# Kernel optimization log

Measured on AMD Instinct MI355X. Metric: run time of the kernel, lower is better.

## Reference

```python
import jax, jax.numpy as jnp
import numpy as np

D_MODEL = 40
NUM_BUCKETS = 32
MAX_DISTANCE = 128
EPS = 1e-6


def rms_norm(x, w):
    # T5 LayerNorm: no mean subtraction, no bias
    var = jnp.mean(jnp.square(x), axis=-1, keepdims=True)
    return x * jax.lax.rsqrt(var + EPS) * w


def relative_position_bucket(rel, num_buckets=NUM_BUCKETS, max_distance=MAX_DISTANCE):
    # bidirectional (encoder) variant of T5's bucketing
    num_buckets = num_buckets // 2
    buckets = (rel > 0).astype(jnp.int32) * num_buckets
    rel = jnp.abs(rel)
    max_exact = num_buckets // 2
    is_small = rel < max_exact
    rel_f = jnp.maximum(rel, 1).astype(jnp.float32)
    large = max_exact + (
        jnp.log(rel_f / max_exact) / np.log(max_distance / max_exact) * (num_buckets - max_exact)
    ).astype(jnp.int32)
    large = jnp.minimum(large, num_buckets - 1)
    return buckets + jnp.where(is_small, rel, large)


def setup_inputs() -> dict:
    key = jax.random.key(0)
    ks = jax.random.split(key, 16)
    B, S, Din, D = 8, 2048, 128, D_MODEL
    w = lambda k, shape: (jax.random.normal(k, shape, dtype=jnp.float32) * 0.02)
    return {
        "embs": jax.random.normal(ks[0], (B, S, Din), dtype=jnp.float32),
        "Wa": w(ks[1], (Din, D)),
        "ba": jnp.zeros((D,), dtype=jnp.float32),
        "ln1": jnp.ones((D,), dtype=jnp.float32),
        "Wq": w(ks[2], (D, D)),
        "Wk": w(ks[3], (D, D)),
        "Wv": w(ks[4], (D, D)),
        "Wo": w(ks[5], (D, D)),
        "ln2": jnp.ones((D,), dtype=jnp.float32),
        "wi": w(ks[6], (D, D)),
        "wo": w(ks[7], (D, D)),
        "lnf": jnp.ones((D,), dtype=jnp.float32),
        "rel_bias": w(ks[8], (NUM_BUCKETS, 1)),  # [num_buckets, n_heads=1]
    }


def reference(embs, Wa, ba, ln1, Wq, Wk, Wv, Wo, ln2, wi, wo, lnf, rel_bias):
    # adapter
    x = jax.nn.relu(embs @ Wa + ba)  # [B,S,D]
    S = x.shape[1]

    # --- self-attention block (1 head, d_kv = d_model, no QK scaling) ---
    h = rms_norm(x, ln1)
    q = h @ Wq  # [B,S,D]
    k = h @ Wk
    v = h @ Wv

    pos = jnp.arange(S)
    rel = pos[None, :] - pos[:, None]           # memory - query, [S,S]
    buckets = relative_position_bucket(rel)      # [S,S]
    pos_bias = rel_bias[buckets][:, :, 0]        # [S,S], head dim squeezed (1 head)

    scores = jnp.einsum("bqd,bkd->bqk", q, k) + pos_bias[None]  # [B,S,S]
    attn = jax.nn.softmax(scores, axis=-1)
    o = jnp.einsum("bqk,bkd->bqd", attn, v) @ Wo
    x = x + o

    # --- feed-forward block ---
    h2 = rms_norm(x, ln2)
    f = jax.nn.relu(h2 @ wi) @ wo
    x = x + f

    return rms_norm(x, lnf)
```

## Files before the change

kernel.cpp:

```cpp
#include <hip/hip_runtime.h>
#include <hip/hip_bf16.h>
#include <math.h>

#define D 40
#define DIN 128
#define S 2048
#define B 8
#define NROWS (B*S)
#define DP 64
#define XSTR 48
#define PSTR 64
#define KSTR 72

typedef __bf16 bf16x8 __attribute__((ext_vector_type(8)));
typedef float f32x16 __attribute__((ext_vector_type(16)));

static __device__ __forceinline__ unsigned short f2bf(float f) {
    unsigned u = __builtin_bit_cast(unsigned, f);
    u += 0x7fff + ((u >> 16) & 1);
    return (unsigned short)(u >> 16);
}
static __device__ __forceinline__ float bf2f(unsigned short h) {
    return __builtin_bit_cast(float, (unsigned)h << 16);
}
static __device__ __forceinline__ bf16x8 ldfrag(const unsigned short* p) {
    return __builtin_bit_cast(bf16x8, *(const uint4*)p);
}
static __device__ __forceinline__ unsigned cvtpk(float lo, float hi) {
    unsigned r;
    asm("v_cvt_pk_bf16_f32 %0, %1, %2" : "=v"(r) : "v"(lo), "v"(hi));
    return r;
}
static __device__ __forceinline__ void plswap(unsigned &a, unsigned &b) {
    asm("v_permlane32_swap_b32 %0, %1" : "+v"(a), "+v"(b));
}

__global__ __launch_bounds__(256) void k0_prep(
    const float* __restrict__ Wa, const float* __restrict__ ba, const float* __restrict__ ln1,
    const float* __restrict__ Wq, const float* __restrict__ Wk, const float* __restrict__ Wv,
    const float* __restrict__ Wo, const float* __restrict__ ln2,
    const float* __restrict__ wi, const float* __restrict__ wo,
    const float* __restrict__ rel_bias,
    unsigned short* __restrict__ waT, unsigned short* __restrict__ wqT,
    unsigned short* __restrict__ wkT, unsigned short* __restrict__ wvT,
    unsigned short* __restrict__ woT, unsigned short* __restrict__ wiT,
    unsigned short* __restrict__ wo2T, float* __restrict__ btab)
{
    int i = blockIdx.x * 256 + threadIdx.x;
    if (i < 64*144) {
        int col = i / 144, k = i - col*144;
        float v = 0.f;
        if (col < D) {
            if (k < DIN) v = Wa[k*D + col];
            else if (k == DIN) v = ba[col];
        }
        waT[i] = f2bf(v);
    }
    if (i < 64*48) {
        int col = i / 48, d = i - col*48;
        bool ok = (col < D && d < D);
        float s1 = ok ? ln1[d] : 0.f;
        float s2 = ok ? ln2[d] : 0.f;
        wqT[i]  = f2bf(ok ? Wq[d*D + col] * s1 : 0.f);
        wkT[i]  = f2bf(ok ? Wk[d*D + col] * s1 : 0.f);
        wvT[i]  = f2bf(ok ? Wv[d*D + col] * s1 : 0.f);
        woT[i]  = f2bf(ok ? Wo[d*D + col]      : 0.f);
        wiT[i]  = f2bf(ok ? wi[d*D + col] * s2 : 0.f);
        wo2T[i] = f2bf(ok ? wo[d*D + col]      : 0.f);
    }
    if (i < 2*S - 1) {
        int rel = i - (S - 1);
        int bucket = (rel > 0) ? 16 : 0;
        int ar = rel < 0 ? -rel : rel;
        int add;
        if (ar < 8) {
            add = ar;
        } else {
            float tt = logf((float)ar * 0.125f) / logf(16.0f) * 8.0f;
            int lg = 8 + (int)tt;
            add = lg < 15 ? lg : 15;
        }
        btab[i] = rel_bias[bucket + add];
    }
}

static __device__ __forceinline__ void repack1(const f32x16& t0, uint4& u0, uint4& u1)
{
    unsigned a0=cvtpk(t0[0],t0[1]),  a1=cvtpk(t0[2],t0[3]),
             a2=cvtpk(t0[4],t0[5]),  a3=cvtpk(t0[6],t0[7]);
    plswap(a0,a2); plswap(a1,a3);
    unsigned b0=cvtpk(t0[8],t0[9]),  b1=cvtpk(t0[10],t0[11]),
             b2=cvtpk(t0[12],t0[13]),b3=cvtpk(t0[14],t0[15]);
    plswap(b0,b2); plswap(b1,b3);
    u0 = (uint4){a0,a1,a2,a3}; u1 = (uint4){b0,b1,b2,b3};
}

__global__ __launch_bounds__(128) void k1_adapter_qkv(
    const float* __restrict__ embs,
    const unsigned short* __restrict__ waT, const unsigned short* __restrict__ wqT,
    const unsigned short* __restrict__ wkT, const unsigned short* __restrict__ wvT,
    unsigned short* __restrict__ xb, unsigned short* __restrict__ qb,
    unsigned short* __restrict__ kbq, unsigned short* __restrict__ vT)
{
    __shared__ __attribute__((aligned(16))) unsigned short sE16[32][136];
    __shared__ unsigned short sX[32][56];
    __shared__ float sSS[2][32];

    const int tid = threadIdx.x;

    {
        int r = tid >> 2;
        int cc = (tid & 3) * 32;
        const float* src = embs + (size_t)(blockIdx.x*32 + r) * DIN + cc;
        #pragma unroll
        for (int i = 0; i < 4; ++i) {
            float4 f0 = *(const float4*)(src + i*8);
            float4 f1 = *(const float4*)(src + i*8 + 4);
            uint4 u = { cvtpk(f0.x, f0.y), cvtpk(f0.z, f0.w),
                        cvtpk(f1.x, f1.y), cvtpk(f1.z, f1.w) };
            *(uint4*)&sE16[r][cc + i*8] = u;
        }
    }
    __syncthreads();

    const int w   = tid >> 6;
    const int l   = tid & 63;
    const int lr  = l & 31, hi = l >> 5;
    const int row = blockIdx.x * 32 + lr;
    const int cb  = w * 32;

    bf16x8 eb[9];
    #pragma unroll
    for (int kk = 0; kk < 8; ++kk) eb[kk] = ldfrag(&sE16[lr][kk*16 + hi*8]);
    {
        uint4 u = { hi == 0 ? 0x3f80u : 0u, 0u, 0u, 0u };
        eb[8] = __builtin_bit_cast(bf16x8, u);
    }

    f32x16 x0 = {0,0,0,0,0,0,0,0,0,0,0,0,0,0,0,0};
    #pragma unroll
    for (int kk = 0; kk < 9; ++kk) {
        bf16x8 a0 = ldfrag(waT + (size_t)(cb + lr)*144 + kk*16 + hi*8);
        x0 = __builtin_amdgcn_mfma_f32_32x32x16_bf16(a0, eb[kk], x0, 0,0,0);
    }

    float ss = 0.f;
    #pragma unroll
    for (int r = 0; r < 16; ++r) {
        x0[r] = fmaxf(x0[r], 0.f);
        ss += x0[r]*x0[r];
    }
    ss += __shfl_xor(ss, 32);
    if (hi == 0) sSS[w][lr] = ss;
    __syncthreads();
    const float inv = rsqrtf((sSS[0][lr] + sSS[1][lr]) * (1.0f/D) + 1e-6f);

    {
        uint4 u0, u1; repack1(x0, u0, u1);
        unsigned short* p = xb + (size_t)row*XSTR;
        *(uint4*)(p + cb + hi*8) = u0;
        if (w == 0) *(uint4*)(p + 16 + hi*8) = u1;
    }

    f32x16 xh;
    #pragma unroll
    for (int r = 0; r < 16; ++r) xh[r] = x0[r] * inv;
    {
        uint4 u0, u1; repack1(xh, u0, u1);
        *(uint4*)(&sX[lr][cb + hi*8]) = u0;
        if (w == 0) *(uint4*)(&sX[lr][16 + hi*8]) = u1;
    }
    __syncthreads();
    bf16x8 hb[3];
    #pragma unroll
    for (int t = 0; t < 3; ++t) hb[t] = ldfrag(&sX[lr][t*16 + hi*8]);

    f32x16 qa={0,0,0,0,0,0,0,0,0,0,0,0,0,0,0,0};
    f32x16 ka={0,0,0,0,0,0,0,0,0,0,0,0,0,0,0,0};
    f32x16 va={0,0,0,0,0,0,0,0,0,0,0,0,0,0,0,0};
    #pragma unroll
    for (int t = 0; t < 3; ++t) {
        bf16x8 h = hb[t];
        qa = __builtin_amdgcn_mfma_f32_32x32x16_bf16(ldfrag(wqT + (size_t)(cb+lr)*48 + t*16 + hi*8), h, qa, 0,0,0);
        ka = __builtin_amdgcn_mfma_f32_32x32x16_bf16(ldfrag(wkT + (size_t)(cb+lr)*48 + t*16 + hi*8), h, ka, 0,0,0);
        va = __builtin_amdgcn_mfma_f32_32x32x16_bf16(ldfrag(wvT + (size_t)(cb+lr)*48 + t*16 + hi*8), h, va, 0,0,0);
    }

    {
        uint4 u0, u1; repack1(qa, u0, u1);
        unsigned short* p = qb + (size_t)row*DP;
        *(uint4*)(p + cb + hi*8) = u0;
        if (w == 0) *(uint4*)(p + 16 + hi*8) = u1;
    }
    {
        uint4 u0, u1; repack1(ka, u0, u1);
        unsigned short* p = kbq + (size_t)row*DP;
        *(uint4*)(p + cb + hi*8) = u0;
        if (w == 0) *(uint4*)(p + 16 + hi*8) = u1;
    }
    #pragma unroll
    for (int r = 0; r < 16; ++r) {
        int col = cb + (r&3) + 8*(r>>2) + 4*hi;
        vT[(size_t)col*NROWS + row] = f2bf(va[r]);
    }
}

__global__ __launch_bounds__(256) void k3_attn_mfma(
    const unsigned short* __restrict__ qb, const unsigned short* __restrict__ kb,
    const unsigned short* __restrict__ vT, const float* __restrict__ btab,
    unsigned short* __restrict__ pob, float* __restrict__ pl, int klen, int nsplit)
{
    __shared__ float sbtw[2176 + 16];
    __shared__ __attribute__((aligned(16))) unsigned short sK[64][KSTR];
    __shared__ __attribute__((aligned(16))) unsigned short sV[64][KSTR];

    const int q0blk = blockIdx.x * 128;
    const int kt0   = blockIdx.z * klen;
    const int woff  = (S-1) + kt0 - q0blk - 127;

    int tid = threadIdx.x;
    for (int i = tid; i < klen + 128; i += 256) {
        int g = woff + i;
        sbtw[i] = btab[g < 0 ? 0 : (g > 4094 ? 4094 : g)];
    }

    const int w  = tid >> 6, l = tid & 63;
    const int lr = l & 31,  hi = l >> 5;
    const int b  = blockIdx.y;
    const int q0 = q0blk + w * 32;

    const unsigned short* qrow = qb + ((size_t)(b*S) + q0 + lr) * DP + hi*8;
    bf16x8 qf0 = ldfrag(qrow);
    bf16x8 qf1 = ldfrag(qrow + 16);
    bf16x8 qf2 = ldfrag(qrow + 32);

    f32x16 of0 = {0,0,0,0,0,0,0,0,0,0,0,0,0,0,0,0};
    f32x16 of1 = {0,0,0,0,0,0,0,0,0,0,0,0,0,0,0,0};
    float el = 0.f;

    const int bb = 127 - w*32 - lr + 4*hi;

    const int srow = tid >> 3;
    const int scol = (tid & 7) * 8;

    auto stageRegs = [&](int kc, uint4& rk0, uint4& rk1, uint4& rv0, uint4& rv1) {
        const unsigned short* src = kb + (size_t)(b*S + kt0 + kc)*DP;
        rk0 = *(const uint4*)(src + (size_t)srow*DP + scol);
        rk1 = *(const uint4*)(src + (size_t)(32 + srow)*DP + scol);
        const unsigned short* vsrc = vT + (size_t)(b*S) + kt0 + kc;
        rv0 = *(const uint4*)(vsrc + (size_t)srow*NROWS + scol);
        rv1 = *(const uint4*)(vsrc + (size_t)(32 + srow)*NROWS + scol);
    };
    auto writeLds = [&](const uint4& rk0, const uint4& rk1, const uint4& rv0, const uint4& rv1) {
        *(uint4*)&sK[srow][scol]      = rk0;
        *(uint4*)&sK[32 + srow][scol] = rk1;
        *(uint4*)&sV[srow][scol]      = rv0;
        *(uint4*)&sV[32 + srow][scol] = rv1;
    };

    auto compute = [&](int ktl, int kloc) {
        bf16x8 kf0 = ldfrag(&sK[kloc + lr][hi*8]);
        bf16x8 kf1 = ldfrag(&sK[kloc + lr][16 + hi*8]);
        bf16x8 kf2 = ldfrag(&sK[kloc + lr][32 + hi*8]);
        f32x16 c = {0,0,0,0,0,0,0,0,0,0,0,0,0,0,0,0};
        c = __builtin_amdgcn_mfma_f32_32x32x16_bf16(kf0, qf0, c, 0,0,0);
        c = __builtin_amdgcn_mfma_f32_32x32x16_bf16(kf1, qf1, c, 0,0,0);
        c = __builtin_amdgcn_mfma_f32_32x32x16_bf16(kf2, qf2, c, 0,0,0);

        float e[16];
        #pragma unroll
        for (int r = 0; r < 16; ++r) {
            float s = c[r] + sbtw[bb + ktl + (r&3) + 8*(r>>2)];
            e[r] = __expf(s);
            el += e[r];
        }
        unsigned a0 = cvtpk(e[0],  e[1]);
        unsigned a1 = cvtpk(e[2],  e[3]);
        unsigned a2 = cvtpk(e[4],  e[5]);
        unsigned a3 = cvtpk(e[6],  e[7]);
        plswap(a0, a2);
        plswap(a1, a3);
        unsigned b0 = cvtpk(e[8],  e[9]);
        unsigned b1 = cvtpk(e[10], e[11]);
        unsigned b2 = cvtpk(e[12], e[13]);
        unsigned b3 = cvtpk(e[14], e[15]);
        plswap(b0, b2);
        plswap(b1, b3);
        uint4 u0 = {a0, a1, a2, a3};
        uint4 u1 = {b0, b1, b2, b3};
        bf16x8 pa0 = __builtin_bit_cast(bf16x8, u0);
        bf16x8 pa1 = __builtin_bit_cast(bf16x8, u1);

        bf16x8 vf0 = ldfrag(&sV[lr][kloc + hi*8]);
        bf16x8 vf1 = ldfrag(&sV[lr][kloc + 16 + hi*8]);
        bf16x8 vf2 = ldfrag(&sV[32 + lr][kloc + hi*8]);
        bf16x8 vf3 = ldfrag(&sV[32 + lr][kloc + 16 + hi*8]);

        of0 = __builtin_amdgcn_mfma_f32_32x32x16_bf16(pa0, vf0, of0, 0,0,0);
        of0 = __builtin_amdgcn_mfma_f32_32x32x16_bf16(pa1, vf1, of0, 0,0,0);
        of1 = __builtin_amdgcn_mfma_f32_32x32x16_bf16(pa0, vf2, of1, 0,0,0);
        of1 = __builtin_amdgcn_mfma_f32_32x32x16_bf16(pa1, vf3, of1, 0,0,0);
    };

    {
        uint4 rk0, rk1, rv0, rv1;
        stageRegs(0, rk0, rk1, rv0, rv1);
        writeLds(rk0, rk1, rv0, rv1);
    }
    __syncthreads();

    for (int kc = 0; kc < klen; kc += 64) {
        const bool more = (kc + 64 < klen);
        uint4 rk0, rk1, rv0, rv1;
        if (more) stageRegs(kc + 64, rk0, rk1, rv0, rv1);
        compute(kc, 0);
        compute(kc + 32, 32);
        if (more) {
            __syncthreads();
            writeLds(rk0, rk1, rv0, rv1);
            __syncthreads();
        }
    }

    el += __shfl_xor(el, 32);

    const size_t rb0 = ((size_t)(b*S + q0) * nsplit + blockIdx.z);
    #pragma unroll
    for (int r = 0; r < 16; ++r) {
        int qr = (r&3) + 8*(r>>2) + 4*hi;
        unsigned short* pr = pob + (rb0 + (size_t)qr * nsplit) * PSTR;
        pr[lr] = f2bf(of0[r]);
        if (lr < 8) pr[32 + lr] = f2bf(of1[r]);
    }
    if (hi == 0) pl[(size_t)blockIdx.z * NROWS + b*S + q0 + lr] = el;
}

__global__ __launch_bounds__(128) void k4_out_ff(
    const unsigned short* __restrict__ xb, const unsigned short* __restrict__ pob,
    const float* __restrict__ pl,
    const unsigned short* __restrict__ woT, const unsigned short* __restrict__ wiT,
    const unsigned short* __restrict__ wo2T, const float* __restrict__ lnf,
    float* __restrict__ out, int nsplit)
{
    __shared__ unsigned short sX[32][56];
    __shared__ float sSS[2][32];

    const int tid = threadIdx.x;
    const int w   = tid >> 6;
    const int l   = tid & 63;
    const int lr  = l & 31, hi = l >> 5;
    const int row = blockIdx.x * 32 + lr;
    const int cb  = w * 32;

    float lsum = 0.f;
    for (int s = 0; s < nsplit; ++s) lsum += pl[(size_t)s*NROWS + row];
    const float linv = 1.0f / lsum;

    float a[3][8];
    #pragma unroll
    for (int t = 0; t < 3; ++t)
        #pragma unroll
        for (int j = 0; j < 8; ++j) a[t][j] = 0.f;
    const unsigned short* prow = pob + (size_t)row * nsplit * PSTR;
    for (int s = 0; s < nsplit; ++s) {
        const unsigned short* pr = prow + (size_t)s * PSTR;
        #pragma unroll
        for (int t = 0; t < 3; ++t) {
            if (t == 2 && hi == 1) continue;
            uint4 u = *(const uint4*)(pr + t*16 + hi*8);
            a[t][0] += bf2f((unsigned short)(u.x)); a[t][1] += bf2f((unsigned short)(u.x >> 16));
            a[t][2] += bf2f((unsigned short)(u.y)); a[t][3] += bf2f((unsigned short)(u.y >> 16));
            a[t][4] += bf2f((unsigned short)(u.z)); a[t][5] += bf2f((unsigned short)(u.z >> 16));
            a[t][6] += bf2f((unsigned short)(u.w)); a[t][7] += bf2f((unsigned short)(u.w >> 16));
        }
    }
    bf16x8 ab[3];
    #pragma unroll
    for (int t = 0; t < 3; ++t) {
        uint4 u = { cvtpk(a[t][0]*linv, a[t][1]*linv), cvtpk(a[t][2]*linv, a[t][3]*linv),
                    cvtpk(a[t][4]*linv, a[t][5]*linv), cvtpk(a[t][6]*linv, a[t][7]*linv) };
        ab[t] = __builtin_bit_cast(bf16x8, u);
    }

    f32x16 c = {0,0,0,0,0,0,0,0,0,0,0,0,0,0,0,0};
    #pragma unroll
    for (int t = 0; t < 3; ++t)
        c = __builtin_amdgcn_mfma_f32_32x32x16_bf16(ldfrag(woT + (size_t)(cb+lr)*48 + t*16 + hi*8), ab[t], c, 0,0,0);

    const unsigned short* xr = xb + (size_t)row*XSTR;
    if (w == 0) {
        #pragma unroll
        for (int rr = 0; rr < 4; ++rr) {
            ushort4 v = *(const ushort4*)(xr + rr*8 + 4*hi);
            c[rr*4+0] += bf2f(v.x); c[rr*4+1] += bf2f(v.y);
            c[rr*4+2] += bf2f(v.z); c[rr*4+3] += bf2f(v.w);
        }
    } else {
        ushort4 v = *(const ushort4*)(xr + 32 + 4*hi);
        c[0] += bf2f(v.x); c[1] += bf2f(v.y); c[2] += bf2f(v.z); c[3] += bf2f(v.w);
    }

    float ss = 0.f;
    #pragma unroll
    for (int r = 0; r < 16; ++r) ss += c[r]*c[r];
    ss += __shfl_xor(ss, 32);
    if (hi == 0) sSS[w][lr] = ss;
    __syncthreads();
    const float inv2 = rsqrtf((sSS[0][lr] + sSS[1][lr]) * (1.0f/D) + 1e-6f);

    f32x16 t0;
    #pragma unroll
    for (int r = 0; r < 16; ++r) t0[r] = c[r]*inv2;
    {
        uint4 u0, u1; repack1(t0, u0, u1);
        *(uint4*)(&sX[lr][cb + hi*8]) = u0;
        if (w == 0) *(uint4*)(&sX[lr][16 + hi*8]) = u1;
    }
    __syncthreads();
    bf16x8 hb[3];
    #pragma unroll
    for (int t = 0; t < 3; ++t) hb[t] = ldfrag(&sX[lr][t*16 + hi*8]);
    __syncthreads();

    f32x16 d = {0,0,0,0,0,0,0,0,0,0,0,0,0,0,0,0};
    #pragma unroll
    for (int t = 0; t < 3; ++t)
        d = __builtin_amdgcn_mfma_f32_32x32x16_bf16(ldfrag(wiT + (size_t)(cb+lr)*48 + t*16 + hi*8), hb[t], d, 0,0,0);
    #pragma unroll
    for (int r = 0; r < 16; ++r) d[r] = fmaxf(d[r], 0.f);
    {
        uint4 u0, u1; repack1(d, u0, u1);
        *(uint4*)(&sX[lr][cb + hi*8]) = u0;
        if (w == 0) *(uint4*)(&sX[lr][16 + hi*8]) = u1;
    }
    __syncthreads();
    bf16x8 fb[3];
    #pragma unroll
    for (int t = 0; t < 3; ++t) fb[t] = ldfrag(&sX[lr][t*16 + hi*8]);

    f32x16 e = {0,0,0,0,0,0,0,0,0,0,0,0,0,0,0,0};
    #pragma unroll
    for (int t = 0; t < 3; ++t)
        e = __builtin_amdgcn_mfma_f32_32x32x16_bf16(ldfrag(wo2T + (size_t)(cb+lr)*48 + t*16 + hi*8), fb[t], e, 0,0,0);
    #pragma unroll
    for (int r = 0; r < 16; ++r) e[r] += c[r];

    float ss2 = 0.f;
    #pragma unroll
    for (int r = 0; r < 16; ++r) ss2 += e[r]*e[r];
    ss2 += __shfl_xor(ss2, 32);
    if (hi == 0) sSS[w][lr] = ss2;
    __syncthreads();
    const float inv3 = rsqrtf((sSS[0][lr] + sSS[1][lr]) * (1.0f/D) + 1e-6f);

    float* orow = out + (size_t)row * D;
    if (w == 0) {
        #pragma unroll
        for (int rr = 0; rr < 4; ++rr) {
            float4 lf = *(const float4*)(lnf + rr*8 + 4*hi);
            float4 v = { e[rr*4+0]*inv3*lf.x, e[rr*4+1]*inv3*lf.y,
                         e[rr*4+2]*inv3*lf.z, e[rr*4+3]*inv3*lf.w };
            *(float4*)(orow + rr*8 + 4*hi) = v;
        }
    } else {
        float4 lf = *(const float4*)(lnf + 32 + 4*hi);
        float4 v = { e[0]*inv3*lf.x, e[1]*inv3*lf.y, e[2]*inv3*lf.z, e[3]*inv3*lf.w };
        *(float4*)(orow + 32 + 4*hi) = v;
    }
}

extern "C" void kernel_launch(void* const* d_in, const int* in_sizes, int n_in,
                              void* d_out, int out_size, void* d_ws, size_t ws_size,
                              hipStream_t stream) {
    const float* embs = (const float*)d_in[0];
    const float* Wa   = (const float*)d_in[1];
    const float* ba   = (const float*)d_in[2];
    const float* ln1  = (const float*)d_in[3];
    const float* Wq   = (const float*)d_in[4];
    const float* Wk   = (const float*)d_in[5];
    const float* Wv   = (const float*)d_in[6];
    const float* Wo   = (const float*)d_in[7];
    const float* ln2  = (const float*)d_in[8];
    const float* wi   = (const float*)d_in[9];
    const float* wo   = (const float*)d_in[10];
    const float* lnf  = (const float*)d_in[11];
    const float* rb   = (const float*)d_in[12];

    char* wsb = (char*)d_ws;
    unsigned short* xb   = (unsigned short*)(wsb);
    unsigned short* qb   = (unsigned short*)(wsb + 1572864);
    unsigned short* kbq  = (unsigned short*)(wsb + 3670016);
    unsigned short* vT   = (unsigned short*)(wsb + 5767168);
    unsigned short* waT  = (unsigned short*)(wsb + 7864320);
    unsigned short* wqT  = (unsigned short*)(wsb + 7882752);
    unsigned short* wkT  = (unsigned short*)(wsb + 7888896);
    unsigned short* wvT  = (unsigned short*)(wsb + 7895040);
    unsigned short* woT  = (unsigned short*)(wsb + 7901184);
    unsigned short* wiT  = (unsigned short*)(wsb + 7907328);
    unsigned short* wo2T = (unsigned short*)(wsb + 7913472);
    const size_t base = 7919616;

    int nsplit = 8;
    while (nsplit > 1 &&
           base + (size_t)nsplit*(2097152 + 65536) + 16384 > ws_size)
        nsplit >>= 1;
    unsigned short* pob = (unsigned short*)(wsb + base);
    float* pl   = (float*)(wsb + base + (size_t)nsplit*2097152);
    float* btab = (float*)(wsb + base + (size_t)nsplit*(2097152 + 65536));
    int klen = S / nsplit;

    k0_prep<<<36, 256, 0, stream>>>(Wa, ba, ln1, Wq, Wk, Wv, Wo, ln2, wi, wo, rb,
                                    waT, wqT, wkT, wvT, woT, wiT, wo2T, btab);
    k1_adapter_qkv<<<NROWS/32, 128, 0, stream>>>(embs, waT, wqT, wkT, wvT, xb, qb, kbq, vT);
    k3_attn_mfma<<<dim3(S/128, B, nsplit), 256, 0, stream>>>(qb, kbq, vT, btab, pob, pl, klen, nsplit);
    k4_out_ff<<<NROWS/32, 128, 0, stream>>>(xb, pob, pl, woT, wiT, wo2T, lnf, (float*)d_out, nsplit);
}
```

Baseline: 45.55 us.

## Process two query tiles per wave in attention kernel to reuse staged K/V

Each attention block now covers 256 query rows instead of 128. Each wave holds two sets of Q fragments and two sets of accumulators and runs both against every K/V tile staged in LDS. This halves the K/V global loads and LDS staging per query and halves the grid size. The cost is more registers per thread, which the launch bound of 2 blocks per CU tries to contain, and fewer blocks (with nsplit=8 it drops from 1024 to 512) to fill the CUs.

```diff
diff --git a/kernel.cpp b/kernel.cpp
--- a/kernel.cpp
+++ b/kernel.cpp
@@ -205,21 +205,21 @@
     }
 }
 
-__global__ __launch_bounds__(256) void k3_attn_mfma(
+__global__ __launch_bounds__(256, 2) void k3_attn_mfma(
     const unsigned short* __restrict__ qb, const unsigned short* __restrict__ kb,
     const unsigned short* __restrict__ vT, const float* __restrict__ btab,
     unsigned short* __restrict__ pob, float* __restrict__ pl, int klen, int nsplit)
 {
-    __shared__ float sbtw[2176 + 16];
+    __shared__ float sbtw[2432];
     __shared__ __attribute__((aligned(16))) unsigned short sK[64][KSTR];
     __shared__ __attribute__((aligned(16))) unsigned short sV[64][KSTR];
 
-    const int q0blk = blockIdx.x * 128;
+    const int q0blk = blockIdx.x * 256;
     const int kt0   = blockIdx.z * klen;
-    const int woff  = (S-1) + kt0 - q0blk - 127;
+    const int woff  = (S-1) + kt0 - q0blk - 255;
 
     int tid = threadIdx.x;
-    for (int i = tid; i < klen + 128; i += 256) {
+    for (int i = tid; i < klen + 256; i += 256) {
         int g = woff + i;
         sbtw[i] = btab[g < 0 ? 0 : (g > 4094 ? 4094 : g)];
     }
@@ -227,18 +227,22 @@
     const int w  = tid >> 6, l = tid & 63;
     const int lr = l & 31,  hi = l >> 5;
     const int b  = blockIdx.y;
-    const int q0 = q0blk + w * 32;
-
-    const unsigned short* qrow = qb + ((size_t)(b*S) + q0 + lr) * DP + hi*8;
-    bf16x8 qf0 = ldfrag(qrow);
-    bf16x8 qf1 = ldfrag(qrow + 16);
-    bf16x8 qf2 = ldfrag(qrow + 32);
-
-    f32x16 of0 = {0,0,0,0,0,0,0,0,0,0,0,0,0,0,0,0};
-    f32x16 of1 = {0,0,0,0,0,0,0,0,0,0,0,0,0,0,0,0};
-    float el = 0.f;
-
-    const int bb = 127 - w*32 - lr + 4*hi;
+    const int q0a = q0blk + w * 32;
+    const int q0b = q0a + 128;
+
+    const unsigned short* qrA = qb + ((size_t)(b*S) + q0a + lr) * DP + hi*8;
+    bf16x8 qfA[3] = { ldfrag(qrA), ldfrag(qrA + 16), ldfrag(qrA + 32) };
+    const unsigned short* qrB = qb + ((size_t)(b*S) + q0b + lr) * DP + hi*8;
+    bf16x8 qfB[3] = { ldfrag(qrB), ldfrag(qrB + 16), ldfrag(qrB + 32) };
+
+    f32x16 oA0 = {0,0,0,0,0,0,0,0,0,0,0,0,0,0,0,0};
+    f32x16 oA1 = {0,0,0,0,0,0,0,0,0,0,0,0,0,0,0,0};
+    f32x16 oB0 = {0,0,0,0,0,0,0,0,0,0,0,0,0,0,0,0};
+    f32x16 oB1 = {0,0,0,0,0,0,0,0,0,0,0,0,0,0,0,0};
+    float elA = 0.f, elB = 0.f;
+
+    const int bbA = 255 - w*32 - lr + 4*hi;
+    const int bbB = bbA - 128;
 
     const int srow = tid >> 3;
     const int scol = (tid & 7) * 8;
@@ -258,14 +262,15 @@
         *(uint4*)&sV[32 + srow][scol] = rv1;
     };
 
-    auto compute = [&](int ktl, int kloc) {
+    auto compute = [&](int ktl, int kloc, const bf16x8* qf,
+                       f32x16& o0, f32x16& o1, float& el, int bb) {
         bf16x8 kf0 = ldfrag(&sK[kloc + lr][hi*8]);
         bf16x8 kf1 = ldfrag(&sK[kloc + lr][16 + hi*8]);
         bf16x8 kf2 = ldfrag(&sK[kloc + lr][32 + hi*8]);
         f32x16 c = {0,0,0,0,0,0,0,0,0,0,0,0,0,0,0,0};
-        c = __builtin_amdgcn_mfma_f32_32x32x16_bf16(kf0, qf0, c, 0,0,0);
-        c = __builtin_amdgcn_mfma_f32_32x32x16_bf16(kf1, qf1, c, 0,0,0);
-        c = __builtin_amdgcn_mfma_f32_32x32x16_bf16(kf2, qf2, c, 0,0,0);
+        c = __builtin_amdgcn_mfma_f32_32x32x16_bf16(kf0, qf[0], c, 0,0,0);
+        c = __builtin_amdgcn_mfma_f32_32x32x16_bf16(kf1, qf[1], c, 0,0,0);
+        c = __builtin_amdgcn_mfma_f32_32x32x16_bf16(kf2, qf[2], c, 0,0,0);
 
         float e[16];
         #pragma unroll
@@ -296,10 +301,10 @@
         bf16x8 vf2 = ldfrag(&sV[32 + lr][kloc + hi*8]);
         bf16x8 vf3 = ldfrag(&sV[32 + lr][kloc + 16 + hi*8]);
 
-        of0 = __builtin_amdgcn_mfma_f32_32x32x16_bf16(pa0, vf0, of0, 0,0,0);
-        of0 = __builtin_amdgcn_mfma_f32_32x32x16_bf16(pa1, vf1, of0, 0,0,0);
-        of1 = __builtin_amdgcn_mfma_f32_32x32x16_bf16(pa0, vf2, of1, 0,0,0);
-        of1 = __builtin_amdgcn_mfma_f32_32x32x16_bf16(pa1, vf3, of1, 0,0,0);
+        o0 = __builtin_amdgcn_mfma_f32_32x32x16_bf16(pa0, vf0, o0, 0,0,0);
+        o0 = __builtin_amdgcn_mfma_f32_32x32x16_bf16(pa1, vf1, o0, 0,0,0);
+        o1 = __builtin_amdgcn_mfma_f32_32x32x16_bf16(pa0, vf2, o1, 0,0,0);
+        o1 = __builtin_amdgcn_mfma_f32_32x32x16_bf16(pa1, vf3, o1, 0,0,0);
     };
 
     {
@@ -313,8 +318,10 @@
         const bool more = (kc + 64 < klen);
         uint4 rk0, rk1, rv0, rv1;
         if (more) stageRegs(kc + 64, rk0, rk1, rv0, rv1);
-        compute(kc, 0);
-        compute(kc + 32, 32);
+        compute(kc,      0,  qfA, oA0, oA1, elA, bbA);
+        compute(kc,      0,  qfB, oB0, oB1, elB, bbB);
+        compute(kc + 32, 32, qfA, oA0, oA1, elA, bbA);
+        compute(kc + 32, 32, qfB, oB0, oB1, elB, bbB);
         if (more) {
             __syncthreads();
             writeLds(rk0, rk1, rv0, rv1);
@@ -322,17 +329,25 @@
         }
     }
 
-    el += __shfl_xor(el, 32);
-
-    const size_t rb0 = ((size_t)(b*S + q0) * nsplit + blockIdx.z);
+    elA += __shfl_xor(elA, 32);
+    elB += __shfl_xor(elB, 32);
+
+    const size_t rbA = ((size_t)(b*S + q0a) * nsplit + blockIdx.z);
+    const size_t rbB = ((size_t)(b*S + q0b) * nsplit + blockIdx.z);
     #pragma unroll
     for (int r = 0; r < 16; ++r) {
         int qr = (r&3) + 8*(r>>2) + 4*hi;
-        unsigned short* pr = pob + (rb0 + (size_t)qr * nsplit) * PSTR;
-        pr[lr] = f2bf(of0[r]);
-        if (lr < 8) pr[32 + lr] = f2bf(of1[r]);
-    }
-    if (hi == 0) pl[(size_t)blockIdx.z * NROWS + b*S + q0 + lr] = el;
+        unsigned short* prA = pob + (rbA + (size_t)qr * nsplit) * PSTR;
+        prA[lr] = f2bf(oA0[r]);
+        if (lr < 8) prA[32 + lr] = f2bf(oA1[r]);
+        unsigned short* prB = pob + (rbB + (size_t)qr * nsplit) * PSTR;
+        prB[lr] = f2bf(oB0[r]);
+        if (lr < 8) prB[32 + lr] = f2bf(oB1[r]);
+    }
+    if (hi == 0) {
+        pl[(size_t)blockIdx.z * NROWS + b*S + q0a + lr] = elA;
+        pl[(size_t)blockIdx.z * NROWS + b*S + q0b + lr] = elB;
+    }
 }
 
 __global__ __launch_bounds__(128) void k4_out_ff(
@@ -512,6 +527,6 @@
     k0_prep<<<36, 256, 0, stream>>>(Wa, ba, ln1, Wq, Wk, Wv, Wo, ln2, wi, wo, rb,
                                     waT, wqT, wkT, wvT, woT, wiT, wo2T, btab);
     k1_adapter_qkv<<<NROWS/32, 128, 0, stream>>>(embs, waT, wqT, wkT, wvT, xb, qb, kbq, vT);
-    k3_attn_mfma<<<dim3(S/128, B, nsplit), 256, 0, stream>>>(qb, kbq, vT, btab, pob, pl, klen, nsplit);
+    k3_attn_mfma<<<dim3(S/256, B, nsplit), 256, 0, stream>>>(qb, kbq, vT, btab, pob, pl, klen, nsplit);
     k4_out_ff<<<NROWS/32, 128, 0, stream>>>(xb, pob, pl, woT, wiT, wo2T, lnf, (float*)d_out, nsplit);
 }
```

Result: no change. 44.86 us (-1.5%).
